# Optimization experiments

Measured on AMD Instinct MI355X. Metric: run time of the kernel, lower is better.

Reference implementation:

```python
import jax, jax.numpy as jnp
import numpy as np

B, NT, NZ, CIN, H, DOUT, L = 16, 128, 256, 3, 64, 128, 3
N = NT * NZ  # 32768 nodes
EPS = 1e-5


def _build_edges():
    # Toroidal grid: each node connects to 4 neighbors (wrap-around in theta and zeta).
    T, Z = np.meshgrid(np.arange(NT), np.arange(NZ), indexing='ij')
    curr = (T * NZ + Z).ravel()
    nbrs = np.stack([
        (((T + 1) % NT) * NZ + Z).ravel(),
        (((T - 1) % NT) * NZ + Z).ravel(),
        (T * NZ + (Z + 1) % NZ).ravel(),
        (T * NZ + (Z - 1) % NZ).ravel(),
    ], axis=1)
    src = np.repeat(curr, 4)
    dst = nbrs.ravel()
    return np.stack([src, dst]).astype(np.int32)  # (2, 4N)


def setup_inputs() -> dict:
    key = jax.random.key(0)
    ks = jax.random.split(key, 8)
    s = lambda k, shp, fan: jax.random.normal(k, shp, jnp.float32) / np.float32(np.sqrt(fan))
    return {
        'x': jax.random.normal(ks[0], (B, CIN, N), jnp.float32),
        'edge_index': jnp.asarray(_build_edges()),
        'embed_W': s(ks[1], (CIN, H), CIN),
        'embed_b': jnp.zeros((H,), jnp.float32),
        'mp_W1': s(ks[2], (L, 2 * H, H), 2 * H),
        'mp_b1': jnp.zeros((L, H), jnp.float32),
        'mp_g1': jnp.ones((L, H), jnp.float32),
        'mp_be1': jnp.zeros((L, H), jnp.float32),
        'mp_W2': s(ks[3], (L, H, H), H),
        'mp_b2': jnp.zeros((L, H), jnp.float32),
        'mp_g2': jnp.ones((L, H), jnp.float32),
        'mp_be2': jnp.zeros((L, H), jnp.float32),
        'head_W1': s(ks[4], (H, H), H),
        'head_b1': jnp.zeros((H,), jnp.float32),
        'head_W2': s(ks[5], (H, DOUT), H),
        'head_b2': jnp.zeros((DOUT,), jnp.float32),
    }


def _bn(y, g, b):
    # BatchNorm1d in training mode: biased batch stats over (batch*nodes).
    m = y.mean(axis=(0, 1))
    v = y.var(axis=(0, 1))
    return (y - m) * (g * jax.lax.rsqrt(v + EPS)) + b


def reference(x, edge_index, embed_W, embed_b, mp_W1, mp_b1, mp_g1, mp_be1,
              mp_W2, mp_b2, mp_g2, mp_be2, head_W1, head_b1, head_W2, head_b2):
    src, dst = edge_index[0], edge_index[1]
    # embedding: (B,3,N) -> (B,N,H)
    h = jax.nn.relu(jnp.einsum('bcn,ch->bnh', x, embed_W) + embed_b)
    deg = jnp.zeros((N,), x.dtype).at[dst].add(1.0)
    deg = jnp.clip(deg, 1.0)[None, :, None]  # (1,N,1), all 4 on this graph
    for l in range(L):
        # gather neighbor features and scatter-add to destination, mean aggregate
        agg = jnp.zeros_like(h).at[:, dst, :].add(h[:, src, :]) / deg
        comb = jnp.concatenate([h, agg], axis=-1)  # (B,N,2H)
        y = jax.nn.relu(_bn(comb @ mp_W1[l] + mp_b1[l], mp_g1[l], mp_be1[l]))
        y = jax.nn.relu(_bn(y @ mp_W2[l] + mp_b2[l], mp_g2[l], mp_be2[l]))
        h = y + h  # residual (c_in == c_out)
    pooled = h.mean(axis=1)  # AdaptiveAvgPool1d(1) over nodes
    return jax.nn.relu(pooled @ head_W1 + head_b1) @ head_W2 + head_b2
```

## Files before the change

kernel.cpp:

```cpp
#include <hip/hip_runtime.h>

typedef unsigned short u16;
typedef u16 u16x8 __attribute__((ext_vector_type(8)));
typedef short s16x8 __attribute__((ext_vector_type(8)));
typedef float f32x4 __attribute__((ext_vector_type(4)));

#define NNODES 32768
#define EPSV 1e-5f
#define INV_ROWS (1.0f / 524288.0f)

__device__ __forceinline__ float bf2f(u16 u) {
  union { unsigned int i; float f; } v; v.i = ((unsigned int)u) << 16; return v.f;
}
__device__ __forceinline__ u16 f2bf(float f) {
  union { float f; unsigned int i; } v; v.f = f;
  unsigned int r = v.i + 0x7FFFu + ((v.i >> 16) & 1u);
  return (u16)(r >> 16);
}

__global__ __launch_bounds__(256) void k_embed(
    const float* __restrict__ x, const float* __restrict__ eW,
    const float* __restrict__ eb, u16* __restrict__ h) {
  int tid = threadIdx.x;
  int chunk = tid & 7;
  int r = blockIdx.x * 32 + (tid >> 3);
  int b = r >> 15;
  int n = r & 32767;
  const float* xb = x + (size_t)b * 3 * NNODES + n;
  float x0 = xb[0], x1 = xb[NNODES], x2 = xb[2 * NNODES];
  int c0 = chunk * 8;
  u16x8 ov;
#pragma unroll
  for (int j = 0; j < 8; ++j) {
    float acc = eb[c0 + j] + x0 * eW[c0 + j] + x1 * eW[64 + c0 + j] + x2 * eW[128 + c0 + j];
    ov[j] = f2bf(fmaxf(acc, 0.f));
  }
  *reinterpret_cast<u16x8*>(&h[(size_t)r * 64 + c0]) = ov;
}

__global__ __launch_bounds__(256) void k_gemm1(
    const u16* __restrict__ h, u16* __restrict__ ybuf,
    const float* __restrict__ W1, const float* __restrict__ b1,
    float* __restrict__ sums) {
  __shared__ __align__(16) u16 w_s[64 * 136];
  __shared__ __align__(16) u16 t_s[4][16 * 72];
  __shared__ float red_s[256], red2_s[256];
  __shared__ float stat_s[128];

  int tid = threadIdx.x;
  int wv = tid >> 6, ln = tid & 63, ln15 = ln & 15, quad = ln >> 4;
  int blk = blockIdx.x;
  int xcd = blk & 7;
  int j = blk >> 3;
  int b = j >> 5;
  int local = j & 31;
  int t = xcd * 16 + (local >> 1);
  int half = local & 1;
  const u16* hb = h + (((size_t)b) << 15) * 64;
  int tp = (t + 1) & 127, tm = (t + 127) & 127;

  for (int idx = tid; idx < 8192; idx += 256) {
    int k = idx >> 6, n = idx & 63;
    float w = W1[idx];
    if (k >= 64) w *= 0.25f;
    w_s[n * 136 + k] = f2bf(w);
  }
  __syncthreads();

  s16x8 bfT[4][2], bfB[4][2];
#pragma unroll
  for (int c = 0; c < 4; ++c)
#pragma unroll
    for (int kk = 0; kk < 2; ++kk) {
      bfT[c][kk] = *reinterpret_cast<const s16x8*>(
          &w_s[(c * 16 + ln15) * 136 + kk * 32 + quad * 8]);
      bfB[c][kk] = *reinterpret_cast<const s16x8*>(
          &w_s[(c * 16 + ln15) * 136 + 64 + kk * 32 + quad * 8]);
    }

  float bias_c[4];
#pragma unroll
  for (int c = 0; c < 4; ++c) bias_c[c] = b1[c * 16 + ln15];

  float ls[4] = {0.f, 0.f, 0.f, 0.f}, ls2[4] = {0.f, 0.f, 0.f, 0.f};
  u16* ts = &t_s[wv][0];

#pragma unroll 1
  for (int st = 0; st < 2; ++st) {
    int z0 = half * 128 + wv * 32 + st * 16;
    int z = z0 + ln15;
    int zp = (z + 1) & 255, zm = (z + 255) & 255;
    size_t rS  = ((size_t)(t * 256 + z)) * 64;
    size_t rTp = ((size_t)(tp * 256 + z)) * 64;
    size_t rTm = ((size_t)(tm * 256 + z)) * 64;
    size_t rZp = ((size_t)(t * 256 + zp)) * 64;
    size_t rZm = ((size_t)(t * 256 + zm)) * 64;
    int cA = quad * 8;

    s16x8 s0  = *reinterpret_cast<const s16x8*>(&hb[rS + cA]);
    s16x8 s1  = *reinterpret_cast<const s16x8*>(&hb[rS + 32 + cA]);
    s16x8 n0a = *reinterpret_cast<const s16x8*>(&hb[rTp + cA]);
    s16x8 n0b = *reinterpret_cast<const s16x8*>(&hb[rTp + 32 + cA]);
    s16x8 n1a = *reinterpret_cast<const s16x8*>(&hb[rTm + cA]);
    s16x8 n1b = *reinterpret_cast<const s16x8*>(&hb[rTm + 32 + cA]);
    s16x8 n2a = *reinterpret_cast<const s16x8*>(&hb[rZp + cA]);
    s16x8 n2b = *reinterpret_cast<const s16x8*>(&hb[rZp + 32 + cA]);
    s16x8 n3a = *reinterpret_cast<const s16x8*>(&hb[rZm + cA]);
    s16x8 n3b = *reinterpret_cast<const s16x8*>(&hb[rZm + 32 + cA]);

    f32x4 acc[4];
#pragma unroll
    for (int c = 0; c < 4; ++c) acc[c] = (f32x4){0.f, 0.f, 0.f, 0.f};
#pragma unroll
    for (int c = 0; c < 4; ++c) {
      acc[c] = __builtin_amdgcn_mfma_f32_16x16x32_bf16(s0,  bfT[c][0], acc[c], 0, 0, 0);
      acc[c] = __builtin_amdgcn_mfma_f32_16x16x32_bf16(s1,  bfT[c][1], acc[c], 0, 0, 0);
      acc[c] = __builtin_amdgcn_mfma_f32_16x16x32_bf16(n0a, bfB[c][0], acc[c], 0, 0, 0);
      acc[c] = __builtin_amdgcn_mfma_f32_16x16x32_bf16(n0b, bfB[c][1], acc[c], 0, 0, 0);
      acc[c] = __builtin_amdgcn_mfma_f32_16x16x32_bf16(n1a, bfB[c][0], acc[c], 0, 0, 0);
      acc[c] = __builtin_amdgcn_mfma_f32_16x16x32_bf16(n1b, bfB[c][1], acc[c], 0, 0, 0);
      acc[c] = __builtin_amdgcn_mfma_f32_16x16x32_bf16(n2a, bfB[c][0], acc[c], 0, 0, 0);
      acc[c] = __builtin_amdgcn_mfma_f32_16x16x32_bf16(n2b, bfB[c][1], acc[c], 0, 0, 0);
      acc[c] = __builtin_amdgcn_mfma_f32_16x16x32_bf16(n3a, bfB[c][0], acc[c], 0, 0, 0);
      acc[c] = __builtin_amdgcn_mfma_f32_16x16x32_bf16(n3b, bfB[c][1], acc[c], 0, 0, 0);
    }

    __builtin_amdgcn_wave_barrier();
#pragma unroll
    for (int c = 0; c < 4; ++c)
#pragma unroll
      for (int rg = 0; rg < 4; ++rg) {
        float vy = acc[c][rg] + bias_c[c];
        ls[c] += vy;
        ls2[c] += vy * vy;
        ts[(quad * 4 + rg) * 72 + c * 16 + ln15] = f2bf(vy);
      }
    __builtin_amdgcn_wave_barrier();
    size_t R0 = (((size_t)b) << 15) + (size_t)t * 256 + z0;
    int lr = ln >> 2;
#pragma unroll
    for (int p = 0; p < 2; ++p) {
      int ck = (ln & 3) + p * 4;
      u16x8 v = *reinterpret_cast<const u16x8*>(&ts[lr * 72 + ck * 8]);
      *reinterpret_cast<u16x8*>(&ybuf[(R0 + lr) * 64 + ck * 8]) = v;
    }
    __builtin_amdgcn_wave_barrier();
  }

#pragma unroll
  for (int c = 0; c < 4; ++c) {
    red_s[tid] = ls[c];
    red2_s[tid] = ls2[c];
    __syncthreads();
    if (tid < 16) {
      float s = 0.f, s2 = 0.f;
#pragma unroll
      for (int g = 0; g < 16; ++g) { s += red_s[g * 16 + tid]; s2 += red2_s[g * 16 + tid]; }
      stat_s[c * 16 + tid] = s;
      stat_s[64 + c * 16 + tid] = s2;
    }
    __syncthreads();
  }
  if (tid < 128) atomicAdd(&sums[xcd * 128 + tid], stat_s[tid]);
}

__global__ __launch_bounds__(256) void k_gemm2(
    u16* __restrict__ ybuf, const float* __restrict__ W2,
    const float* __restrict__ b2, const float* __restrict__ sums1,
    const float* __restrict__ g1, const float* __restrict__ be1,
    float* __restrict__ sums2) {
  __shared__ __align__(16) u16 w_s[64 * 72];
  __shared__ __align__(16) u16 t_s[4][16 * 72];
  __shared__ float s1_s[64], sh1_s[64];
  __shared__ float red_s[256], red2_s[256];
  __shared__ float stat_s[128];

  int tid = threadIdx.x;
  int wv = tid >> 6, ln = tid & 63, ln15 = ln & 15, quad = ln >> 4;

  if (tid < 64) {
    float s = 0.f, s2 = 0.f;
#pragma unroll
    for (int sl = 0; sl < 8; ++sl) { s += sums1[sl * 128 + tid]; s2 += sums1[sl * 128 + 64 + tid]; }
    float m = s * INV_ROWS;
    float v = s2 * INV_ROWS - m * m;
    float sc = g1[tid] * rsqrtf(v + EPSV);
    s1_s[tid] = sc;
    sh1_s[tid] = be1[tid] - m * sc;
  }
  for (int idx = tid; idx < 4096; idx += 256) {
    int k = idx >> 6, n = idx & 63;
    w_s[n * 72 + k] = f2bf(W2[idx]);
  }
  __syncthreads();

  s16x8 bf[4][2];
#pragma unroll
  for (int c = 0; c < 4; ++c)
#pragma unroll
    for (int kk = 0; kk < 2; ++kk)
      bf[c][kk] = *reinterpret_cast<const s16x8*>(
          &w_s[(c * 16 + ln15) * 72 + kk * 32 + quad * 8]);

  float sA[2][8], shA[2][8];
#pragma unroll
  for (int kk = 0; kk < 2; ++kk)
#pragma unroll
    for (int j = 0; j < 8; ++j) {
      int ch = kk * 32 + quad * 8 + j;
      sA[kk][j] = s1_s[ch];
      shA[kk][j] = sh1_s[ch];
    }

  float bias_c[4];
#pragma unroll
  for (int c = 0; c < 4; ++c) bias_c[c] = b2[c * 16 + ln15];

  float ls[4] = {0.f, 0.f, 0.f, 0.f}, ls2[4] = {0.f, 0.f, 0.f, 0.f};
  u16* ts = &t_s[wv][0];

#pragma unroll 1
  for (int st = 0; st < 2; ++st) {
    size_t r0 = (size_t)blockIdx.x * 128 + wv * 32 + st * 16;
    size_t row = r0 + ln15;
    u16x8 y0 = *reinterpret_cast<const u16x8*>(&ybuf[row * 64 + quad * 8]);
    u16x8 y1 = *reinterpret_cast<const u16x8*>(&ybuf[row * 64 + 32 + quad * 8]);
    s16x8 a0, a1;
#pragma unroll
    for (int j = 0; j < 8; ++j) {
      a0[j] = (short)f2bf(fmaxf(bf2f(y0[j]) * sA[0][j] + shA[0][j], 0.f));
      a1[j] = (short)f2bf(fmaxf(bf2f(y1[j]) * sA[1][j] + shA[1][j], 0.f));
    }

    f32x4 acc[4];
#pragma unroll
    for (int c = 0; c < 4; ++c) acc[c] = (f32x4){0.f, 0.f, 0.f, 0.f};
#pragma unroll
    for (int c = 0; c < 4; ++c) {
      acc[c] = __builtin_amdgcn_mfma_f32_16x16x32_bf16(a0, bf[c][0], acc[c], 0, 0, 0);
      acc[c] = __builtin_amdgcn_mfma_f32_16x16x32_bf16(a1, bf[c][1], acc[c], 0, 0, 0);
    }

    __builtin_amdgcn_wave_barrier();
#pragma unroll
    for (int c = 0; c < 4; ++c)
#pragma unroll
      for (int rg = 0; rg < 4; ++rg) {
        float vy = acc[c][rg] + bias_c[c];
        ls[c] += vy;
        ls2[c] += vy * vy;
        ts[(quad * 4 + rg) * 72 + c * 16 + ln15] = f2bf(vy);
      }
    __builtin_amdgcn_wave_barrier();
    int lr = ln >> 2;
#pragma unroll
    for (int p = 0; p < 2; ++p) {
      int ck = (ln & 3) + p * 4;
      u16x8 v = *reinterpret_cast<const u16x8*>(&ts[lr * 72 + ck * 8]);
      *reinterpret_cast<u16x8*>(&ybuf[(r0 + lr) * 64 + ck * 8]) = v;
    }
    __builtin_amdgcn_wave_barrier();
  }

#pragma unroll
  for (int c = 0; c < 4; ++c) {
    red_s[tid] = ls[c];
    red2_s[tid] = ls2[c];
    __syncthreads();
    if (tid < 16) {
      float s = 0.f, s2 = 0.f;
#pragma unroll
      for (int g = 0; g < 16; ++g) { s += red_s[g * 16 + tid]; s2 += red2_s[g * 16 + tid]; }
      stat_s[c * 16 + tid] = s;
      stat_s[64 + c * 16 + tid] = s2;
    }
    __syncthreads();
  }
  if (tid < 128) atomicAdd(&sums2[(blockIdx.x & 7) * 128 + tid], stat_s[tid]);
}

__global__ __launch_bounds__(256) void k_resid(
    u16* __restrict__ h, const u16* __restrict__ zbuf,
    const float* __restrict__ sums2, const float* __restrict__ g2,
    const float* __restrict__ be2, float* __restrict__ pooled) {
  __shared__ float s2_s[64], sh2_s[64];
  __shared__ float red_s[32][68];
  int tid = threadIdx.x;
  if (tid < 64) {
    float s = 0.f, s2 = 0.f;
#pragma unroll
    for (int sl = 0; sl < 8; ++sl) { s += sums2[sl * 128 + tid]; s2 += sums2[sl * 128 + 64 + tid]; }
    float m = s * INV_ROWS;
    float v = s2 * INV_ROWS - m * m;
    float sc = g2[tid] * rsqrtf(v + EPSV);
    s2_s[tid] = sc;
    sh2_s[tid] = be2[tid] - m * sc;
  }
  __syncthreads();
  int ch0 = (tid & 7) * 8;
  float scl[8], shl[8];
#pragma unroll
  for (int j = 0; j < 8; ++j) { scl[j] = s2_s[ch0 + j]; shl[j] = sh2_s[ch0 + j]; }
  float p[8] = {0.f, 0.f, 0.f, 0.f, 0.f, 0.f, 0.f, 0.f};
  size_t base0 = (size_t)blockIdx.x * 16384 + tid * 8;
#pragma unroll 1
  for (int it = 0; it < 8; ++it) {
    size_t base = base0 + it * 2048;
    u16x8 zv = *reinterpret_cast<const u16x8*>(&zbuf[base]);
    u16x8 hv = *reinterpret_cast<const u16x8*>(&h[base]);
    u16x8 ov;
#pragma unroll
    for (int j = 0; j < 8; ++j) {
      float a = fmaxf(bf2f(zv[j]) * scl[j] + shl[j], 0.f);
      float nh = bf2f(hv[j]) + a;
      ov[j] = f2bf(nh);
      p[j] += bf2f(ov[j]);
    }
    *reinterpret_cast<u16x8*>(&h[base]) = ov;
  }
  if (pooled != nullptr) {
    int g = tid >> 3;
#pragma unroll
    for (int j = 0; j < 8; ++j) red_s[g][ch0 + j] = p[j];
    __syncthreads();
    if (tid < 64) {
      float s = 0.f;
#pragma unroll
      for (int gg = 0; gg < 32; ++gg) s += red_s[gg][tid];
      atomicAdd(&pooled[(blockIdx.x >> 7) * 64 + tid], s);
    }
  }
}

__global__ __launch_bounds__(256) void k_head(
    const float* __restrict__ pooled, const float* __restrict__ hW1,
    const float* __restrict__ hb1, const float* __restrict__ hW2,
    const float* __restrict__ hb2, float* __restrict__ out) {
  __shared__ float p_s[16 * 64];
  __shared__ float t1_s[16 * 64];
  int tid = threadIdx.x;
#pragma unroll
  for (int j = 0; j < 4; ++j)
    p_s[tid + 256 * j] = pooled[tid + 256 * j] * (1.0f / 32768.0f);
  __syncthreads();
#pragma unroll
  for (int j = 0; j < 4; ++j) {
    int idx = tid + 256 * j;
    int bb = idx >> 6, o = idx & 63;
    float acc = hb1[o];
    for (int k = 0; k < 64; ++k) acc += p_s[bb * 64 + k] * hW1[k * 64 + o];
    t1_s[idx] = fmaxf(acc, 0.f);
  }
  __syncthreads();
#pragma unroll
  for (int j = 0; j < 8; ++j) {
    int idx = tid + 256 * j;
    int bb = idx >> 7, o = idx & 127;
    float acc = hb2[o];
    for (int k = 0; k < 64; ++k) acc += t1_s[bb * 64 + k] * hW2[k * 128 + o];
    out[idx] = acc;
  }
}

extern "C" void kernel_launch(void* const* d_in, const int* in_sizes, int n_in,
                              void* d_out, int out_size, void* d_ws, size_t ws_size,
                              hipStream_t stream) {
  const float* x   = (const float*)d_in[0];
  const float* eW  = (const float*)d_in[2];
  const float* eb  = (const float*)d_in[3];
  const float* W1  = (const float*)d_in[4];
  const float* b1  = (const float*)d_in[5];
  const float* g1  = (const float*)d_in[6];
  const float* be1 = (const float*)d_in[7];
  const float* W2  = (const float*)d_in[8];
  const float* b2  = (const float*)d_in[9];
  const float* g2  = (const float*)d_in[10];
  const float* be2 = (const float*)d_in[11];
  const float* hW1 = (const float*)d_in[12];
  const float* hb1 = (const float*)d_in[13];
  const float* hW2 = (const float*)d_in[14];
  const float* hb2 = (const float*)d_in[15];
  float* out = (float*)d_out;

  char* ws = (char*)d_ws;
  u16* h    = (u16*)ws;
  u16* ybuf = (u16*)(ws + 67108864);
  float* stats  = (float*)(ws + 134217728);
  float* pooled = stats + 6144;

  hipMemsetAsync(stats, 0, (6144 + 1024) * sizeof(float), stream);

  k_embed<<<16384, 256, 0, stream>>>(x, eW, eb, h);
  for (int l = 0; l < 3; ++l) {
    float* sum1 = stats + l * 2048;
    float* sum2 = stats + l * 2048 + 1024;
    k_gemm1<<<4096, 256, 0, stream>>>(h, ybuf, W1 + l * 8192, b1 + l * 64, sum1);
    k_gemm2<<<4096, 256, 0, stream>>>(ybuf, W2 + l * 4096, b2 + l * 64,
                                      sum1, g1 + l * 64, be1 + l * 64, sum2);
    k_resid<<<2048, 256, 0, stream>>>(h, ybuf, sum2, g2 + l * 64, be2 + l * 64,
                                      (l == 2) ? pooled : nullptr);
  }
  k_head<<<1, 256, 0, stream>>>(pooled, hW1, hb1, hW2, hb2, out);
}
```

Measured before the change: 495.8 us.

## Process more rows per block in GEMM kernels and use shuffle-based stat reduction

Each GEMM block now handles 512 rows in 8 iterations instead of 128 rows in 2, with grid sizes cut from 4096 to 1024. This amortizes the per-block weight staging into LDS and the fragment loads over four times more work. The batch-norm statistics reduction now uses wave shuffles plus a single barrier instead of eight block-wide barriers. The trade-off is fewer blocks in flight, which leaves less parallelism to hide memory latency.

```diff
diff --git a/kernel.cpp b/kernel.cpp
--- a/kernel.cpp
+++ b/kernel.cpp
@@ -44,20 +44,17 @@
     float* __restrict__ sums) {
   __shared__ __align__(16) u16 w_s[64 * 136];
   __shared__ __align__(16) u16 t_s[4][16 * 72];
-  __shared__ float red_s[256], red2_s[256];
-  __shared__ float stat_s[128];
+  __shared__ float stat_s[4][128];
 
   int tid = threadIdx.x;
   int wv = tid >> 6, ln = tid & 63, ln15 = ln & 15, quad = ln >> 4;
   int blk = blockIdx.x;
   int xcd = blk & 7;
   int j = blk >> 3;
-  int b = j >> 5;
-  int local = j & 31;
-  int t = xcd * 16 + (local >> 1);
-  int half = local & 1;
+  int b = j >> 3;
+  int local = j & 7;
+  int tbase = (xcd * 8 + local) * 2;
   const u16* hb = h + (((size_t)b) << 15) * 64;
-  int tp = (t + 1) & 127, tm = (t + 127) & 127;
 
   for (int idx = tid; idx < 8192; idx += 256) {
     int k = idx >> 6, n = idx & 63;
@@ -84,10 +81,13 @@
 
   float ls[4] = {0.f, 0.f, 0.f, 0.f}, ls2[4] = {0.f, 0.f, 0.f, 0.f};
   u16* ts = &t_s[wv][0];
+  int cA = quad * 8;
 
 #pragma unroll 1
-  for (int st = 0; st < 2; ++st) {
-    int z0 = half * 128 + wv * 32 + st * 16;
+  for (int it = 0; it < 8; ++it) {
+    int t = tbase + (it >> 2);
+    int tp = (t + 1) & 127, tm = (t + 127) & 127;
+    int z0 = (it & 3) * 64 + wv * 16;
     int z = z0 + ln15;
     int zp = (z + 1) & 255, zm = (z + 255) & 255;
     size_t rS  = ((size_t)(t * 256 + z)) * 64;
@@ -95,7 +95,6 @@
     size_t rTm = ((size_t)(tm * 256 + z)) * 64;
     size_t rZp = ((size_t)(t * 256 + zp)) * 64;
     size_t rZm = ((size_t)(t * 256 + zm)) * 64;
-    int cA = quad * 8;
 
     s16x8 s0  = *reinterpret_cast<const s16x8*>(&hb[rS + cA]);
     s16x8 s1  = *reinterpret_cast<const s16x8*>(&hb[rS + 32 + cA]);
@@ -149,19 +148,21 @@
 
 #pragma unroll
   for (int c = 0; c < 4; ++c) {
-    red_s[tid] = ls[c];
-    red2_s[tid] = ls2[c];
-    __syncthreads();
-    if (tid < 16) {
-      float s = 0.f, s2 = 0.f;
-#pragma unroll
-      for (int g = 0; g < 16; ++g) { s += red_s[g * 16 + tid]; s2 += red2_s[g * 16 + tid]; }
-      stat_s[c * 16 + tid] = s;
-      stat_s[64 + c * 16 + tid] = s2;
-    }
-    __syncthreads();
-  }
-  if (tid < 128) atomicAdd(&sums[xcd * 128 + tid], stat_s[tid]);
+    ls[c]  += __shfl_xor(ls[c], 16, 64);  ls[c]  += __shfl_xor(ls[c], 32, 64);
+    ls2[c] += __shfl_xor(ls2[c], 16, 64); ls2[c] += __shfl_xor(ls2[c], 32, 64);
+  }
+  if (ln < 16) {
+#pragma unroll
+    for (int c = 0; c < 4; ++c) {
+      stat_s[wv][c * 16 + ln] = ls[c];
+      stat_s[wv][64 + c * 16 + ln] = ls2[c];
+    }
+  }
+  __syncthreads();
+  if (tid < 128) {
+    float s = stat_s[0][tid] + stat_s[1][tid] + stat_s[2][tid] + stat_s[3][tid];
+    atomicAdd(&sums[xcd * 128 + tid], s);
+  }
 }
 
 __global__ __launch_bounds__(256) void k_gemm2(
@@ -172,8 +173,7 @@
   __shared__ __align__(16) u16 w_s[64 * 72];
   __shared__ __align__(16) u16 t_s[4][16 * 72];
   __shared__ float s1_s[64], sh1_s[64];
-  __shared__ float red_s[256], red2_s[256];
-  __shared__ float stat_s[128];
+  __shared__ float stat_s[4][128];
 
   int tid = threadIdx.x;
   int wv = tid >> 6, ln = tid & 63, ln15 = ln & 15, quad = ln >> 4;
@@ -220,8 +220,8 @@
   u16* ts = &t_s[wv][0];
 
 #pragma unroll 1
-  for (int st = 0; st < 2; ++st) {
-    size_t r0 = (size_t)blockIdx.x * 128 + wv * 32 + st * 16;
+  for (int it = 0; it < 8; ++it) {
+    size_t r0 = (size_t)blockIdx.x * 512 + it * 64 + wv * 16;
     size_t row = r0 + ln15;
     u16x8 y0 = *reinterpret_cast<const u16x8*>(&ybuf[row * 64 + quad * 8]);
     u16x8 y1 = *reinterpret_cast<const u16x8*>(&ybuf[row * 64 + 32 + quad * 8]);
@@ -264,19 +264,21 @@
 
 #pragma unroll
   for (int c = 0; c < 4; ++c) {
-    red_s[tid] = ls[c];
-    red2_s[tid] = ls2[c];
-    __syncthreads();
-    if (tid < 16) {
-      float s = 0.f, s2 = 0.f;
-#pragma unroll
-      for (int g = 0; g < 16; ++g) { s += red_s[g * 16 + tid]; s2 += red2_s[g * 16 + tid]; }
-      stat_s[c * 16 + tid] = s;
-      stat_s[64 + c * 16 + tid] = s2;
-    }
-    __syncthreads();
-  }
-  if (tid < 128) atomicAdd(&sums2[(blockIdx.x & 7) * 128 + tid], stat_s[tid]);
+    ls[c]  += __shfl_xor(ls[c], 16, 64);  ls[c]  += __shfl_xor(ls[c], 32, 64);
+    ls2[c] += __shfl_xor(ls2[c], 16, 64); ls2[c] += __shfl_xor(ls2[c], 32, 64);
+  }
+  if (ln < 16) {
+#pragma unroll
+    for (int c = 0; c < 4; ++c) {
+      stat_s[wv][c * 16 + ln] = ls[c];
+      stat_s[wv][64 + c * 16 + ln] = ls2[c];
+    }
+  }
+  __syncthreads();
+  if (tid < 128) {
+    float s = stat_s[0][tid] + stat_s[1][tid] + stat_s[2][tid] + stat_s[3][tid];
+    atomicAdd(&sums2[(blockIdx.x & 7) * 128 + tid], s);
+  }
 }
 
 __global__ __launch_bounds__(256) void k_resid(
@@ -394,8 +396,8 @@
   for (int l = 0; l < 3; ++l) {
     float* sum1 = stats + l * 2048;
     float* sum2 = stats + l * 2048 + 1024;
-    k_gemm1<<<4096, 256, 0, stream>>>(h, ybuf, W1 + l * 8192, b1 + l * 64, sum1);
-    k_gemm2<<<4096, 256, 0, stream>>>(ybuf, W2 + l * 4096, b2 + l * 64,
+    k_gemm1<<<1024, 256, 0, stream>>>(h, ybuf, W1 + l * 8192, b1 + l * 64, sum1);
+    k_gemm2<<<1024, 256, 0, stream>>>(ybuf, W2 + l * 4096, b2 + l * 64,
                                       sum1, g1 + l * 64, be1 + l * 64, sum2);
     k_resid<<<2048, 256, 0, stream>>>(h, ybuf, sum2, g2 + l * 64, be2 + l * 64,
                                       (l == 2) ? pooled : nullptr);
```

After: 489.7 us. About the same (-1.2%).
